# Kernel optimization log

Measured on AMD Instinct MI355X. Metric: run time of the kernel, lower is better.

The kernel has to match this reference:

```python
import jax, jax.numpy as jnp
import numpy as np

B, N, HID, NH = 8, 1024, 1024, 16
HD = HID // NH  # head_dim = 64
MLP = 4 * HID
EPS = 1e-6


def _xavier(key, fan_in, fan_out):
    lim = np.sqrt(6.0 / (fan_in + fan_out))
    return jax.random.uniform(key, (fan_in, fan_out), jnp.float32, -lim, lim)


def setup_inputs() -> dict:
    key = jax.random.key(0)
    ks = jax.random.split(key, 10)
    return {
        "x": jax.random.normal(ks[0], (B, N, HID), jnp.float32),
        "c": jax.random.normal(ks[1], (B, HID), jnp.float32),
        "w_ada": _xavier(ks[2], HID, 6 * HID), "b_ada": jnp.zeros((6 * HID,), jnp.float32),
        "wq": _xavier(ks[3], HID, HID), "bq": jnp.zeros((HID,), jnp.float32),
        "wk": _xavier(ks[4], HID, HID), "bk": jnp.zeros((HID,), jnp.float32),
        "wv": _xavier(ks[5], HID, HID), "bv": jnp.zeros((HID,), jnp.float32),
        "wo": _xavier(ks[6], HID, HID), "bo": jnp.zeros((HID,), jnp.float32),
        "w1": _xavier(ks[7], HID, MLP), "b1": jnp.zeros((MLP,), jnp.float32),
        "w2": _xavier(ks[8], MLP, HID), "b2": jnp.zeros((HID,), jnp.float32),
    }


def _ln(t):
    # LayerNorm, elementwise_affine=False, eps=1e-6
    mu = jnp.mean(t, axis=-1, keepdims=True)
    var = jnp.mean(jnp.square(t - mu), axis=-1, keepdims=True)
    return (t - mu) * jax.lax.rsqrt(var + EPS)


def _modulate(t, shift, scale):
    return t * (1.0 + scale[:, None, :]) + shift[:, None, :]


def reference(x, c, w_ada, b_ada, wq, bq, wk, bk, wv, bv, wo, bo, w1, b1, w2, b2):
    cmod = jax.nn.silu(c) @ w_ada + b_ada  # [B, 6*HID]
    sh_msa, sc_msa, g_msa, sh_mlp, sc_mlp, g_mlp = jnp.split(cmod, 6, axis=-1)

    xm = _modulate(_ln(x), sh_msa, sc_msa)  # [B, N, HID]
    q = (xm @ wq + bq).reshape(B, N, NH, HD)
    k = (xm @ wk + bk).reshape(B, N, NH, HD)
    v = (xm @ wv + bv).reshape(B, N, NH, HD)

    # NOTE: original scales by 1/head_dim (not 1/sqrt(head_dim)), fp32 softmax
    scores = jnp.einsum('bihd,bjhd->bhij', q, k) / HD
    attn = jax.nn.softmax(scores.astype(jnp.float32), axis=-1)
    out = jnp.einsum('bhij,bjhd->bihd', attn, v).astype(v.dtype)
    out = out.reshape(B, N, HID) @ wo + bo

    x = x + g_msa[:, None, :] * out

    xm2 = _modulate(_ln(x), sh_mlp, sc_mlp)
    h = jax.nn.gelu(xm2 @ w1 + b1, approximate=False)  # nn.GELU default = exact
    mlp_out = h @ w2 + b2
    return x + g_mlp[:, None, :] * mlp_out
```

## Files before the change

kernel.cpp:

```cpp
#include <hip/hip_runtime.h>
#include <hip/hip_bf16.h>
#include <cstdint>


typedef __bf16 bf16;
typedef __attribute__((ext_vector_type(8))) __bf16 bf16x8;
typedef __attribute__((ext_vector_type(4))) __bf16 bf16x4;
typedef __attribute__((ext_vector_type(4))) float f32x4;

#define SEQ   1024
#define NHID  1024
#define NHEAD 16
#define HDIM  64
#define CMS   6144

#define GLD16(gp, lp)                                                  \
  __builtin_amdgcn_global_load_lds(                                    \
      (const __attribute__((address_space(1))) void*)(gp),             \
      (__attribute__((address_space(3))) void*)(lp), 16, 0, 0)

template <int N> __device__ __forceinline__ void vmwait() {
  if constexpr (N == 0)      asm volatile("s_waitcnt vmcnt(0)" ::: "memory");
  else if constexpr (N == 3) asm volatile("s_waitcnt vmcnt(3)" ::: "memory");
  else if constexpr (N == 4) asm volatile("s_waitcnt vmcnt(4)" ::: "memory");
  else if constexpr (N == 6) asm volatile("s_waitcnt vmcnt(6)" ::: "memory");
  else                       asm volatile("s_waitcnt vmcnt(8)" ::: "memory");
}

struct TP4 { const float* s[4]; bf16* d[4]; };

__global__ __launch_bounds__(256) void transpose_conv4(TP4 p)
{
  __shared__ float tile[32][33];
  const float* __restrict__ src = p.s[blockIdx.z];
  bf16* __restrict__ dst = p.d[blockIdx.z];
  int n0 = blockIdx.x * 32, k0 = blockIdx.y * 32;
  int tx = threadIdx.x & 31, ty = threadIdx.x >> 5;
#pragma unroll
  for (int i = 0; i < 32; i += 8)
    tile[ty + i][tx] = src[(size_t)(k0 + ty + i) * 1024 + n0 + tx];
  __syncthreads();
#pragma unroll
  for (int i = 0; i < 32; i += 8)
    dst[(size_t)(n0 + ty + i) * 1024 + k0 + tx] = (bf16)tile[tx][ty + i];
}

__global__ __launch_bounds__(256) void transpose_conv(
    const float* __restrict__ src, bf16* __restrict__ dst, int K, int N)
{
  __shared__ float tile[32][33];
  int n0 = blockIdx.x * 32, k0 = blockIdx.y * 32;
  int tx = threadIdx.x & 31, ty = threadIdx.x >> 5;
#pragma unroll
  for (int i = 0; i < 32; i += 8)
    tile[ty + i][tx] = src[(size_t)(k0 + ty + i) * N + n0 + tx];
  __syncthreads();
#pragma unroll
  for (int i = 0; i < 32; i += 8)
    dst[(size_t)(n0 + ty + i) * K + k0 + tx] = (bf16)tile[tx][ty + i];
}

__global__ __launch_bounds__(256) void ada_kernel(
    const float* __restrict__ c, const float* __restrict__ w_ada,
    const float* __restrict__ b_ada, float* __restrict__ cmod)
{
  __shared__ float cs[1024];
  int b = blockIdx.y;
  int col = blockIdx.x * 256 + threadIdx.x;
  for (int i = threadIdx.x; i < 1024; i += 256) {
    float cv = c[b * 1024 + i];
    cs[i] = cv / (1.0f + __expf(-cv));
  }
  __syncthreads();
  float acc = b_ada[col];
#pragma unroll 8
  for (int kk = 0; kk < 1024; kk++)
    acc += cs[kk] * w_ada[(size_t)kk * CMS + col];
  cmod[b * CMS + col] = acc;
}

__global__ __launch_bounds__(256) void ln_mod(
    const float* __restrict__ x, const float* __restrict__ cmod,
    bf16* __restrict__ out, int sh_off, int sc_off)
{
  int row = blockIdx.x, b = row >> 10, tid = threadIdx.x;
  const float4* xr = (const float4*)(x + (size_t)row * NHID);
  float4 v = xr[tid];
  float s  = v.x + v.y + v.z + v.w;
  float s2 = v.x * v.x + v.y * v.y + v.z * v.z + v.w * v.w;
#pragma unroll
  for (int off = 32; off; off >>= 1) {
    s  += __shfl_xor(s, off);
    s2 += __shfl_xor(s2, off);
  }
  __shared__ float red1[4], red2[4];
  int wave = tid >> 6, lane = tid & 63;
  if (lane == 0) { red1[wave] = s; red2[wave] = s2; }
  __syncthreads();
  float S  = red1[0] + red1[1] + red1[2] + red1[3];
  float S2 = red2[0] + red2[1] + red2[2] + red2[3];
  float mean = S * (1.0f / NHID);
  float var  = S2 * (1.0f / NHID) - mean * mean;
  float rs   = rsqrtf(var + 1e-6f);
  const float4* shp = (const float4*)(cmod + b * CMS + sh_off);
  const float4* scp = (const float4*)(cmod + b * CMS + sc_off);
  float4 sh4 = shp[tid], sc4 = scp[tid];
  bf16x4 o4;
  o4[0] = (bf16)((v.x - mean) * rs * (1.0f + sc4.x) + sh4.x);
  o4[1] = (bf16)((v.y - mean) * rs * (1.0f + sc4.y) + sh4.y);
  o4[2] = (bf16)((v.z - mean) * rs * (1.0f + sc4.z) + sh4.z);
  o4[3] = (bf16)((v.w - mean) * rs * (1.0f + sc4.w) + sh4.w);
  *(bf16x4*)(out + (size_t)row * NHID + tid * 4) = o4;
}

template <int EPI, int BN>
__global__ __launch_bounds__(512, 2) void gemm8(
    const bf16* __restrict__ A, const bf16* __restrict__ Bt,
    const float* __restrict__ bias, const float* __restrict__ bias2,
    const float* __restrict__ bias3,
    bf16* __restrict__ outb, bf16* __restrict__ outb2,
    bf16* __restrict__ outb3, float* __restrict__ outf,
    const float* __restrict__ cmod, int gate_off,
    const float* __restrict__ resid,
    int N, int K)
{
  constexpr int BNH   = BN / 2;
  constexpr int LB    = BNH / 64;
  constexpr int NF    = BN / 128;
  constexpr int VMS   = 4 + 2 * LB;
  constexpr int VMF   = 2 + LB;
  constexpr int BOFF  = 65536;
  constexpr int BBUF  = BNH * 256;
  constexpr int BHALF = BNH * 128;

  extern __shared__ __align__(16) char smem[];

  const int tid  = threadIdx.x;
  const int bm = blockIdx.y * 256, bn = blockIdx.x * BN;
  const int wave = tid >> 6, lane = tid & 63;
  const int wr = wave >> 2, wc = wave & 3;
  const int l16 = lane & 15, q4 = lane >> 4;

  const int rq = tid >> 3;
  const int ch = ((tid & 7) ^ (rq & 7)) * 8;
  const int wbase = (tid & 448) * 16;

  const int aRowB = (wr * 64 + l16) * 128;
  const int bRowB = (wc * (BN >> 3) + l16) * 128;
  const int slotB = (q4 ^ (l16 & 7)) * 16;

  f32x4 acc[2][2][4][NF];
#pragma unroll
  for (int a0 = 0; a0 < 2; a0++)
#pragma unroll
    for (int a1 = 0; a1 < 2; a1++)
#pragma unroll
      for (int a2 = 0; a2 < 4; a2++)
#pragma unroll
        for (int a3 = 0; a3 < NF; a3++) acc[a0][a1][a2][a3] = (f32x4)0.0f;

  auto stA = [&](int buf, int half, int T) {
    const bf16* g = A + (size_t)(bm + half * 128 + rq) * K + T * 64 + ch;
    char* l = smem + buf * 32768 + half * 16384 + wbase;
    GLD16(g, l);
    GLD16(g + (size_t)64 * K, l + 8192);
  };
  auto stB = [&](int buf, int half, int T) {
    const bf16* g = Bt + (size_t)(bn + half * BNH + rq) * K + T * 64 + ch;
    char* l = smem + BOFF + buf * BBUF + half * BHALF + wbase;
    GLD16(g, l);
    if constexpr (LB == 2) { GLD16(g + (size_t)64 * K, l + 8192); }
  };

#define PHASE(VMN, BUF, QM, QN, ...)                                       \
  {                                                                        \
    vmwait<VMN>();                                                         \
    __builtin_amdgcn_s_barrier();                                          \
    asm volatile("" ::: "memory");                                         \
    __VA_ARGS__                                                            \
    const char* ab = smem + (BUF) * 32768 + (QM) * 16384 + aRowB;          \
    const char* bb = smem + BOFF + (BUF) * BBUF + (QN) * BHALF + bRowB;    \
    bf16x8 afr[2][4]; bf16x8 bfr[2][NF];                                   \
    _Pragma("unroll")                                                      \
    for (int ks = 0; ks < 2; ks++) {                                       \
      const int sb = slotB ^ (ks * 64);                                    \
      _Pragma("unroll")                                                    \
      for (int mf = 0; mf < 4; mf++)                                       \
        afr[ks][mf] = *(const bf16x8*)(ab + mf * 2048 + sb);               \
      _Pragma("unroll")                                                    \
      for (int nf = 0; nf < NF; nf++)                                      \
        bfr[ks][nf] = *(const bf16x8*)(bb + nf * 2048 + sb);               \
    }                                                                      \
    __builtin_amdgcn_s_setprio(1);                                         \
    _Pragma("unroll")                                                      \
    for (int mf = 0; mf < 4; mf++)                                         \
      _Pragma("unroll")                                                    \
      for (int nf = 0; nf < NF; nf++) {                                    \
        acc[QM][QN][mf][nf] = __builtin_amdgcn_mfma_f32_16x16x32_bf16(     \
            afr[0][mf], bfr[0][nf], acc[QM][QN][mf][nf], 0, 0, 0);         \
        acc[QM][QN][mf][nf] = __builtin_amdgcn_mfma_f32_16x16x32_bf16(     \
            afr[1][mf], bfr[1][nf], acc[QM][QN][mf][nf], 0, 0, 0);         \
      }                                                                    \
    __builtin_amdgcn_s_setprio(0);                                         \
  }

  const int NT = K >> 6, NI = NT >> 1;

  stA(0, 0, 0); stB(0, 0, 0);
  stA(0, 1, 0); stB(0, 1, 0);
  stA(1, 0, 1); stB(1, 0, 1);

  for (int i = 0; i < NI - 1; ++i) {
    const int t = 2 * i;
    PHASE(VMS, 0, 0, 0, stA(1, 1, t + 1); stB(1, 1, t + 1);)
    PHASE(VMS, 0, 0, 1, ;)
    PHASE(VMS, 0, 1, 0, stA(0, 0, t + 2);)
    PHASE(VMS, 0, 1, 1, stB(0, 0, t + 2);)
    PHASE(VMS, 1, 0, 0, stA(0, 1, t + 2); stB(0, 1, t + 2);)
    PHASE(VMS, 1, 0, 1, ;)
    PHASE(VMS, 1, 1, 0, stA(1, 0, t + 3);)
    PHASE(VMS, 1, 1, 1, stB(1, 0, t + 3);)
  }
  {
    const int t = NT - 2;
    PHASE(VMS, 0, 0, 0, stA(1, 1, t + 1); stB(1, 1, t + 1);)
    PHASE(VMS, 0, 0, 1, ;)
    PHASE(VMS, 0, 1, 0, ;)
    PHASE(VMS, 0, 1, 1, ;)
    PHASE(VMF, 1, 0, 0, ;)
    PHASE(0,   1, 0, 1, ;)
    PHASE(0,   1, 1, 0, ;)
    PHASE(0,   1, 1, 1, ;)
  }
#undef PHASE

  const int colBase = bn + wc * (BN >> 3) + l16;
  const int rowBase = bm + wr * 64 + q4 * 4;
#pragma unroll
  for (int qm = 0; qm < 2; qm++)
#pragma unroll
  for (int qn = 0; qn < 2; qn++)
#pragma unroll
  for (int mf = 0; mf < 4; mf++)
#pragma unroll
  for (int nf = 0; nf < NF; nf++) {
    const int col  = colBase + qn * BNH + nf * 16;
    const int row0 = rowBase + qm * 128 + mf * 16;
    f32x4 v = acc[qm][qn][mf][nf];
    if constexpr (EPI == 5) {
      const int sel = bn >> 10;
      const float* bp = (sel == 0) ? bias : (sel == 1) ? bias2 : bias3;
      const int colq = col & 1023;
      const float bcol = bp[colq];
      if (sel == 2) {
        bf16x4 o4;
#pragma unroll
        for (int r = 0; r < 4; r++) o4[r] = (bf16)(v[r] + bcol);
        const int bidx = row0 >> 10;
        *(bf16x4*)(outb3 + ((size_t)bidx * NHID + colq) * SEQ +
                   (row0 & 1023)) = o4;
      } else {
        bf16* qk = (sel == 0) ? outb : outb2;
#pragma unroll
        for (int r = 0; r < 4; r++)
          qk[(size_t)(row0 + r) * 1024 + colq] = (bf16)(v[r] + bcol);
      }
    } else if constexpr (EPI == 2) {
      const float bcol = bias[col];
#pragma unroll
      for (int r = 0; r < 4; r++) {
        float val = v[r] + bcol;
        float u2 = 2.0f * val * (0.7978845608f + 0.0356774081f * val * val);
        float e = __expf(u2);
        float th = 1.0f - 2.0f / (e + 1.0f);
        outb[(size_t)(row0 + r) * N + col] = (bf16)(0.5f * val * (1.0f + th));
      }
    } else {
      const float bcol = bias[col];
#pragma unroll
      for (int r = 0; r < 4; r++) {
        const int row = row0 + r;
        const float gg = cmod[(row >> 10) * CMS + gate_off + col];
        outf[(size_t)row * N + col] =
            resid[(size_t)row * N + col] + gg * (v[r] + bcol);
      }
    }
  }
}

__global__ __launch_bounds__(256) void attn_mfma(
    const bf16* __restrict__ q, const bf16* __restrict__ k,
    const bf16* __restrict__ vt, bf16* __restrict__ o)
{
  __shared__ __align__(16) bf16 Ks[64 * 64];
  __shared__ __align__(16) bf16 Vs[64 * 64];
  __shared__ __align__(16) bf16 Ps[4][32 * 72];

  int bid = blockIdx.x;
  int qt = bid & 7, h = (bid >> 3) & 15, b = bid >> 7;
  int tid = threadIdx.x, wave = tid >> 6, lane = tid & 63;
  int quad = lane >> 4, l16 = lane & 15;
  int qbase = qt * 128 + wave * 32;

  bf16x8 qf[2][2];
  const bf16* qp = q + ((size_t)(b * SEQ + qbase)) * NHID + h * HDIM;
#pragma unroll
  for (int nt = 0; nt < 2; nt++)
#pragma unroll
    for (int kk = 0; kk < 2; kk++) {
      bf16x8 t = *(const bf16x8*)(qp + (size_t)(nt * 16 + l16) * NHID +
                                  kk * 32 + quad * 8);
#pragma unroll
      for (int j = 0; j < 8; j++) t[j] = (bf16)((float)t[j] * 0.015625f);
      qf[nt][kk] = t;
    }

  f32x4 oacc[4][2];
#pragma unroll
  for (int mt = 0; mt < 4; mt++)
#pragma unroll
    for (int nt = 0; nt < 2; nt++) oacc[mt][nt] = (f32x4)0.0f;
  float m_[2] = {-3.0e38f, -3.0e38f}, l_[2] = {0.0f, 0.0f};

  const bf16* kb = k + ((size_t)(b * SEQ)) * NHID + h * HDIM;
  const bf16* vb = vt + ((size_t)(b * NHID + h * HDIM)) * SEQ;

  const int sr0 = tid >> 3, sc0 = tid & 7;

  for (int kt = 0; kt < 16; kt++) {
    __syncthreads();
#pragma unroll
    for (int i = 0; i < 2; i++) {
      int r = i * 32 + sr0;
      int cg = (sc0 ^ (r & 7)) * 8;
      bf16* lk = Ks + (size_t)(i * 256 + (tid & 192)) * 8;
      bf16* lv = Vs + (size_t)(i * 256 + (tid & 192)) * 8;
      GLD16(kb + (size_t)(kt * 64 + r) * NHID + cg, lk);
      GLD16(vb + (size_t)r * SEQ + kt * 64 + cg, lv);
    }
    __syncthreads();

    f32x4 sacc[4][2];
#pragma unroll
    for (int mt = 0; mt < 4; mt++)
#pragma unroll
      for (int nt = 0; nt < 2; nt++) sacc[mt][nt] = (f32x4)0.0f;
#pragma unroll
    for (int kk = 0; kk < 2; kk++) {
      bf16x8 kf[4];
#pragma unroll
      for (int mt = 0; mt < 4; mt++) {
        int row = mt * 16 + l16;
        kf[mt] = *(const bf16x8*)(Ks + row * 64 +
                                  (((kk * 4 + quad) ^ (row & 7)) * 8));
      }
#pragma unroll
      for (int mt = 0; mt < 4; mt++)
#pragma unroll
        for (int nt = 0; nt < 2; nt++)
          sacc[mt][nt] = __builtin_amdgcn_mfma_f32_16x16x32_bf16(
              kf[mt], qf[nt][kk], sacc[mt][nt], 0, 0, 0);
    }

    float alpha[2];
#pragma unroll
    for (int nt = 0; nt < 2; nt++) {
      float tm = -3.0e38f;
#pragma unroll
      for (int mt = 0; mt < 4; mt++)
#pragma unroll
        for (int r = 0; r < 4; r++) tm = fmaxf(tm, sacc[mt][nt][r]);
      tm = fmaxf(tm, __shfl_xor(tm, 16));
      tm = fmaxf(tm, __shfl_xor(tm, 32));
      float mn = fmaxf(m_[nt], tm);
      alpha[nt] = __expf(m_[nt] - mn);
      m_[nt] = mn;
      float ts = 0.0f;
#pragma unroll
      for (int mt = 0; mt < 4; mt++) {
        bf16x4 pv;
#pragma unroll
        for (int r = 0; r < 4; r++) {
          float p = __expf(sacc[mt][nt][r] - mn);
          ts += p;
          pv[r] = (bf16)p;
        }
        *(bf16x4*)(&Ps[wave][(nt * 16 + l16) * 72 + mt * 16 + quad * 4]) = pv;
      }
      ts += __shfl_xor(ts, 16);
      ts += __shfl_xor(ts, 32);
      l_[nt] = l_[nt] * alpha[nt] + ts;
    }
#pragma unroll
    for (int mt = 0; mt < 4; mt++)
#pragma unroll
      for (int nt = 0; nt < 2; nt++)
#pragma unroll
        for (int r = 0; r < 4; r++) oacc[mt][nt][r] *= alpha[nt];

    __asm__ volatile("s_waitcnt lgkmcnt(0)" ::: "memory");

#pragma unroll
    for (int kk = 0; kk < 2; kk++) {
      bf16x8 vf[4], pf[2];
#pragma unroll
      for (int mt = 0; mt < 4; mt++) {
        int row = mt * 16 + l16;
        vf[mt] = *(const bf16x8*)(Vs + row * 64 +
                                  (((kk * 4 + quad) ^ (row & 7)) * 8));
      }
#pragma unroll
      for (int nt = 0; nt < 2; nt++)
        pf[nt] = *(const bf16x8*)(&Ps[wave][(nt * 16 + l16) * 72 +
                                            kk * 32 + quad * 8]);
#pragma unroll
      for (int mt = 0; mt < 4; mt++)
#pragma unroll
        for (int nt = 0; nt < 2; nt++)
          oacc[mt][nt] = __builtin_amdgcn_mfma_f32_16x16x32_bf16(
              vf[mt], pf[nt], oacc[mt][nt], 0, 0, 0);
    }
  }

#pragma unroll
  for (int nt = 0; nt < 2; nt++) {
    float rl = 1.0f / l_[nt];
#pragma unroll
    for (int mt = 0; mt < 4; mt++) {
      bf16x4 o4;
#pragma unroll
      for (int r = 0; r < 4; r++) o4[r] = (bf16)(oacc[mt][nt][r] * rl);
      *(bf16x4*)(o + ((size_t)(b * SEQ + qbase + nt * 16 + l16)) * NHID +
                 h * HDIM + mt * 16 + quad * 4) = o4;
    }
  }
}

#define OFF_CMOD 0u
#define OFF_WQT  196608u
#define OFF_WKT  (OFF_WQT + 2097152u)
#define OFF_WVT  (OFF_WKT + 2097152u)
#define OFF_WOT  (OFF_WVT + 2097152u)
#define OFF_W1T  (OFF_WOT + 2097152u)
#define OFF_W2T  (OFF_W1T + 8388608u)
#define OFF_X2   (OFF_W2T + 8388608u)
#define OFF_XM2  (OFF_X2  + 33554432u)
#define OFF_POOL (OFF_XM2 + 16777216u)

extern "C" void kernel_launch(void* const* d_in, const int* in_sizes, int n_in,
                              void* d_out, int out_size, void* d_ws, size_t ws_size,
                              hipStream_t stream)
{
  const float* x     = (const float*)d_in[0];
  const float* c     = (const float*)d_in[1];
  const float* w_ada = (const float*)d_in[2];
  const float* b_ada = (const float*)d_in[3];
  const float* wq = (const float*)d_in[4];  const float* bq = (const float*)d_in[5];
  const float* wk = (const float*)d_in[6];  const float* bk = (const float*)d_in[7];
  const float* wv = (const float*)d_in[8];  const float* bv = (const float*)d_in[9];
  const float* wo = (const float*)d_in[10]; const float* bo = (const float*)d_in[11];
  const float* w1 = (const float*)d_in[12]; const float* b1 = (const float*)d_in[13];
  const float* w2 = (const float*)d_in[14]; const float* b2 = (const float*)d_in[15];
  float* out = (float*)d_out;
  char* ws = (char*)d_ws;

  float* cmod = (float*)(ws + OFF_CMOD);
  bf16* wqT = (bf16*)(ws + OFF_WQT);
  bf16* wkT = (bf16*)(ws + OFF_WKT);
  bf16* wvT = (bf16*)(ws + OFF_WVT);
  bf16* woT = (bf16*)(ws + OFF_WOT);
  bf16* w1T = (bf16*)(ws + OFF_W1T);
  bf16* w2T = (bf16*)(ws + OFF_W2T);
  float* x2 = (float*)(ws + OFF_X2);
  bf16* xm2 = (bf16*)(ws + OFF_XM2);
  bf16* xm  = (bf16*)(ws + OFF_POOL);
  bf16* qb  = (bf16*)(ws + OFF_POOL + 16777216u);
  bf16* kb  = (bf16*)(ws + OFF_POOL + 33554432u);
  bf16* vtb = (bf16*)(ws + OFF_POOL + 50331648u);
  bf16* ob  = xm;
  bf16* hb  = xm;

  static bool attr_set = false;
  if (!attr_set) {
    hipFuncSetAttribute(reinterpret_cast<const void*>(&gemm8<5, 128>),
                        hipFuncAttributeMaxDynamicSharedMemorySize, 131072);
    hipFuncSetAttribute(reinterpret_cast<const void*>(&gemm8<1, 128>),
                        hipFuncAttributeMaxDynamicSharedMemorySize, 131072);
    hipFuncSetAttribute(reinterpret_cast<const void*>(&gemm8<2, 256>),
                        hipFuncAttributeMaxDynamicSharedMemorySize, 131072);
    hipFuncSetAttribute(reinterpret_cast<const void*>(&gemm8<3, 128>),
                        hipFuncAttributeMaxDynamicSharedMemorySize, 131072);
    attr_set = true;
  }

  TP4 tp;
  tp.s[0] = wq; tp.s[1] = wk; tp.s[2] = wv; tp.s[3] = wo;
  tp.d[0] = wqT; tp.d[1] = wkT; tp.d[2] = wvT; tp.d[3] = woT;
  transpose_conv4<<<dim3(32, 32, 4), 256, 0, stream>>>(tp);
  transpose_conv<<<dim3(128, 32), 256, 0, stream>>>(w1, w1T, 1024, 4096);
  transpose_conv<<<dim3(32, 128), 256, 0, stream>>>(w2, w2T, 4096, 1024);

  ada_kernel<<<dim3(24, 8), 256, 0, stream>>>(c, w_ada, b_ada, cmod);

  ln_mod<<<8192, 256, 0, stream>>>(x, cmod, xm, 0, 1024);

  gemm8<5, 128><<<dim3(24, 32), 512, 98304, stream>>>(
      xm, wqT, bq, bk, bv, qb, kb, vtb, nullptr, nullptr, 0, nullptr,
      1024, 1024);

  attn_mfma<<<1024, 256, 0, stream>>>(qb, kb, vtb, ob);

  gemm8<1, 128><<<dim3(8, 32), 512, 98304, stream>>>(
      ob, woT, bo, nullptr, nullptr, nullptr, nullptr, nullptr, x2,
      cmod, 2048, x, 1024, 1024);

  ln_mod<<<8192, 256, 0, stream>>>(x2, cmod, xm2, 3072, 4096);

  gemm8<2, 256><<<dim3(16, 32), 512, 131072, stream>>>(
      xm2, w1T, b1, nullptr, nullptr, hb, nullptr, nullptr, nullptr,
      nullptr, 0, nullptr, 4096, 1024);

  gemm8<3, 128><<<dim3(8, 32), 512, 98304, stream>>>(
      hb, w2T, b2, nullptr, nullptr, nullptr, nullptr, nullptr, out,
      cmod, 5120, x2, 1024, 4096);
}
```

Measured before the change: 616.6 us.

## Restructure GEMM main loop to reuse LDS fragments across quadrants and relayout waves

Rewrites the gemm8 pipeline so that A and B fragments read from LDS are reused across consecutive quadrant MFMA groups (0,0 -> 0,1 -> 1,1 -> 1,0), which cuts LDS reads per tile. Prefetch stores now go out between the compute quadrants of a single uniform loop, replacing the peeled tail. The wave grid changes to BN/64 columns, giving each wave 32 columns and MF rows. To keep the loop uniform, the last iterations issue dummy loads of tile 0. This adds redundant global traffic and changes the vmcnt accounting, and the dynamic shared memory attribute for the BN=128 variants is lowered to 98304.

```diff
diff --git a/kernel.cpp b/kernel.cpp
--- a/kernel.cpp
+++ b/kernel.cpp
@@ -21,11 +21,14 @@
 
 template <int N> __device__ __forceinline__ void vmwait() {
   if constexpr (N == 0)      asm volatile("s_waitcnt vmcnt(0)" ::: "memory");
-  else if constexpr (N == 3) asm volatile("s_waitcnt vmcnt(3)" ::: "memory");
-  else if constexpr (N == 4) asm volatile("s_waitcnt vmcnt(4)" ::: "memory");
+  else if constexpr (N == 5) asm volatile("s_waitcnt vmcnt(5)" ::: "memory");
   else if constexpr (N == 6) asm volatile("s_waitcnt vmcnt(6)" ::: "memory");
-  else                       asm volatile("s_waitcnt vmcnt(8)" ::: "memory");
-}
+}
+
+#define BAR()                                                          \
+  { asm volatile("" ::: "memory");                                     \
+    __builtin_amdgcn_s_barrier();                                      \
+    asm volatile("" ::: "memory"); }
 
 struct TP4 { const float* s[4]; bf16* d[4]; };
 
@@ -126,9 +129,10 @@
 {
   constexpr int BNH   = BN / 2;
   constexpr int LB    = BNH / 64;
-  constexpr int NF    = BN / 128;
-  constexpr int VMS   = 4 + 2 * LB;
-  constexpr int VMF   = 2 + LB;
+  constexpr int MF    = BN / 64;
+  constexpr int WC    = BN / 64;
+  constexpr int WRS   = MF * 16;
+  constexpr int VMN   = (LB == 2) ? 6 : 5;
   constexpr int BOFF  = 65536;
   constexpr int BBUF  = BNH * 256;
   constexpr int BHALF = BNH * 128;
@@ -138,26 +142,26 @@
   const int tid  = threadIdx.x;
   const int bm = blockIdx.y * 256, bn = blockIdx.x * BN;
   const int wave = tid >> 6, lane = tid & 63;
-  const int wr = wave >> 2, wc = wave & 3;
+  const int wr = wave / WC, wc = wave % WC;
   const int l16 = lane & 15, q4 = lane >> 4;
 
   const int rq = tid >> 3;
   const int ch = ((tid & 7) ^ (rq & 7)) * 8;
   const int wbase = (tid & 448) * 16;
 
-  const int aRowB = (wr * 64 + l16) * 128;
-  const int bRowB = (wc * (BN >> 3) + l16) * 128;
+  const int aRowB = (wr * WRS + l16) * 128;
+  const int bRowB = (wc * 32 + l16) * 128;
   const int slotB = (q4 ^ (l16 & 7)) * 16;
 
-  f32x4 acc[2][2][4][NF];
+  f32x4 acc[2][2][MF][2];
 #pragma unroll
   for (int a0 = 0; a0 < 2; a0++)
 #pragma unroll
     for (int a1 = 0; a1 < 2; a1++)
 #pragma unroll
-      for (int a2 = 0; a2 < 4; a2++)
-#pragma unroll
-        for (int a3 = 0; a3 < NF; a3++) acc[a0][a1][a2][a3] = (f32x4)0.0f;
+      for (int a2 = 0; a2 < MF; a2++)
+#pragma unroll
+        for (int a3 = 0; a3 < 2; a3++) acc[a0][a1][a2][a3] = (f32x4)0.0f;
 
   auto stA = [&](int buf, int half, int T) {
     const bf16* g = A + (size_t)(bm + half * 128 + rq) * K + T * 64 + ch;
@@ -172,78 +176,94 @@
     if constexpr (LB == 2) { GLD16(g + (size_t)64 * K, l + 8192); }
   };
 
-#define PHASE(VMN, BUF, QM, QN, ...)                                       \
-  {                                                                        \
-    vmwait<VMN>();                                                         \
-    __builtin_amdgcn_s_barrier();                                          \
-    asm volatile("" ::: "memory");                                         \
-    __VA_ARGS__                                                            \
-    const char* ab = smem + (BUF) * 32768 + (QM) * 16384 + aRowB;          \
-    const char* bb = smem + BOFF + (BUF) * BBUF + (QN) * BHALF + bRowB;    \
-    bf16x8 afr[2][4]; bf16x8 bfr[2][NF];                                   \
+#define RDA(BUF, QM, FR)                                                   \
+  { const char* ab_ = smem + (BUF) * 32768 + (QM) * 16384 + aRowB;         \
     _Pragma("unroll")                                                      \
     for (int ks = 0; ks < 2; ks++) {                                       \
-      const int sb = slotB ^ (ks * 64);                                    \
+      const int sb_ = slotB ^ (ks * 64);                                   \
       _Pragma("unroll")                                                    \
-      for (int mf = 0; mf < 4; mf++)                                       \
-        afr[ks][mf] = *(const bf16x8*)(ab + mf * 2048 + sb);               \
+      for (int mf = 0; mf < MF; mf++)                                      \
+        FR[ks][mf] = *(const bf16x8*)(ab_ + mf * 2048 + sb_);              \
+    } }
+
+#define RDB(BUF, QN, FR)                                                   \
+  { const char* bb_ = smem + BOFF + (BUF) * BBUF + (QN) * BHALF + bRowB;   \
+    _Pragma("unroll")                                                      \
+    for (int ks = 0; ks < 2; ks++) {                                       \
+      const int sb_ = slotB ^ (ks * 64);                                   \
       _Pragma("unroll")                                                    \
-      for (int nf = 0; nf < NF; nf++)                                      \
-        bfr[ks][nf] = *(const bf16x8*)(bb + nf * 2048 + sb);               \
-    }                                                                      \
-    __builtin_amdgcn_s_setprio(1);                                         \
+      for (int nf = 0; nf < 2; nf++)                                       \
+        FR[ks][nf] = *(const bf16x8*)(bb_ + nf * 2048 + sb_);              \
+    } }
+
+#define MM(QM, QN, AF, BF)                                                 \
+  { __builtin_amdgcn_s_setprio(1);                                         \
     _Pragma("unroll")                                                      \
-    for (int mf = 0; mf < 4; mf++)                                         \
+    for (int mf = 0; mf < MF; mf++)                                        \
       _Pragma("unroll")                                                    \
-      for (int nf = 0; nf < NF; nf++) {                                    \
+      for (int nf = 0; nf < 2; nf++) {                                     \
         acc[QM][QN][mf][nf] = __builtin_amdgcn_mfma_f32_16x16x32_bf16(     \
-            afr[0][mf], bfr[0][nf], acc[QM][QN][mf][nf], 0, 0, 0);         \
+            AF[0][mf], BF[0][nf], acc[QM][QN][mf][nf], 0, 0, 0);           \
         acc[QM][QN][mf][nf] = __builtin_amdgcn_mfma_f32_16x16x32_bf16(     \
-            afr[1][mf], bfr[1][nf], acc[QM][QN][mf][nf], 0, 0, 0);         \
+            AF[1][mf], BF[1][nf], acc[QM][QN][mf][nf], 0, 0, 0);           \
       }                                                                    \
-    __builtin_amdgcn_s_setprio(0);                                         \
-  }
+    __builtin_amdgcn_s_setprio(0); }
 
   const int NT = K >> 6, NI = NT >> 1;
 
-  stA(0, 0, 0); stB(0, 0, 0);
-  stA(0, 1, 0); stB(0, 1, 0);
-  stA(1, 0, 1); stB(1, 0, 1);
-
-  for (int i = 0; i < NI - 1; ++i) {
+  bf16x8 afr[2][MF], bfr0[2][2], bfr1[2][2];
+
+  stA(0, 0, 0); stB(0, 0, 0); stB(0, 1, 0); stA(0, 1, 0);
+  stA(1, 0, 1); stB(1, 0, 1); stB(1, 1, 1); stA(1, 1, 1);
+
+  for (int i = 0; i < NI; ++i) {
     const int t = 2 * i;
-    PHASE(VMS, 0, 0, 0, stA(1, 1, t + 1); stB(1, 1, t + 1);)
-    PHASE(VMS, 0, 0, 1, ;)
-    PHASE(VMS, 0, 1, 0, stA(0, 0, t + 2);)
-    PHASE(VMS, 0, 1, 1, stB(0, 0, t + 2);)
-    PHASE(VMS, 1, 0, 0, stA(0, 1, t + 2); stB(0, 1, t + 2);)
-    PHASE(VMS, 1, 0, 1, ;)
-    PHASE(VMS, 1, 1, 0, stA(1, 0, t + 3);)
-    PHASE(VMS, 1, 1, 1, stB(1, 0, t + 3);)
-  }
-  {
-    const int t = NT - 2;
-    PHASE(VMS, 0, 0, 0, stA(1, 1, t + 1); stB(1, 1, t + 1);)
-    PHASE(VMS, 0, 0, 1, ;)
-    PHASE(VMS, 0, 1, 0, ;)
-    PHASE(VMS, 0, 1, 1, ;)
-    PHASE(VMF, 1, 0, 0, ;)
-    PHASE(0,   1, 0, 1, ;)
-    PHASE(0,   1, 1, 0, ;)
-    PHASE(0,   1, 1, 1, ;)
-  }
-#undef PHASE
-
-  const int colBase = bn + wc * (BN >> 3) + l16;
-  const int rowBase = bm + wr * 64 + q4 * 4;
+    const int u2 = (t + 2 < NT) ? t + 2 : 0;
+    const int u3 = (t + 3 < NT) ? t + 3 : 0;
+    vmwait<VMN>(); BAR();
+    RDA(0, 0, afr); RDB(0, 0, bfr0);
+    MM(0, 0, afr, bfr0);
+    BAR();
+    RDB(0, 1, bfr1);
+    stA(0, 0, u2); stB(0, 0, u2);
+    MM(0, 1, afr, bfr1);
+    BAR();
+    RDA(0, 1, afr);
+    stB(0, 1, u2);
+    MM(1, 1, afr, bfr1);
+    BAR();
+    stA(0, 1, u2);
+    MM(1, 0, afr, bfr0);
+    vmwait<VMN>(); BAR();
+    RDA(1, 0, afr); RDB(1, 0, bfr0);
+    MM(0, 0, afr, bfr0);
+    BAR();
+    RDB(1, 1, bfr1);
+    stA(1, 0, u3); stB(1, 0, u3);
+    MM(0, 1, afr, bfr1);
+    BAR();
+    RDA(1, 1, afr);
+    stB(1, 1, u3);
+    MM(1, 1, afr, bfr1);
+    BAR();
+    stA(1, 1, u3);
+    MM(1, 0, afr, bfr0);
+  }
+  vmwait<0>();
+#undef RDA
+#undef RDB
+#undef MM
+
+  const int colBase = bn + wc * 32 + l16;
+  const int rowBase = bm + wr * WRS + q4 * 4;
 #pragma unroll
   for (int qm = 0; qm < 2; qm++)
 #pragma unroll
   for (int qn = 0; qn < 2; qn++)
 #pragma unroll
-  for (int mf = 0; mf < 4; mf++)
-#pragma unroll
-  for (int nf = 0; nf < NF; nf++) {
+  for (int mf = 0; mf < MF; mf++)
+#pragma unroll
+  for (int nf = 0; nf < 2; nf++) {
     const int col  = colBase + qn * BNH + nf * 16;
     const int row0 = rowBase + qm * 128 + mf * 16;
     f32x4 v = acc[qm][qn][mf][nf];
@@ -270,8 +290,8 @@
 #pragma unroll
       for (int r = 0; r < 4; r++) {
         float val = v[r] + bcol;
-        float u2 = 2.0f * val * (0.7978845608f + 0.0356774081f * val * val);
-        float e = __expf(u2);
+        float u2g = 2.0f * val * (0.7978845608f + 0.0356774081f * val * val);
+        float e = __expf(u2g);
         float th = 1.0f - 2.0f / (e + 1.0f);
         outb[(size_t)(row0 + r) * N + col] = (bf16)(0.5f * val * (1.0f + th));
       }
@@ -483,13 +503,13 @@
   static bool attr_set = false;
   if (!attr_set) {
     hipFuncSetAttribute(reinterpret_cast<const void*>(&gemm8<5, 128>),
-                        hipFuncAttributeMaxDynamicSharedMemorySize, 131072);
+                        hipFuncAttributeMaxDynamicSharedMemorySize, 98304);
     hipFuncSetAttribute(reinterpret_cast<const void*>(&gemm8<1, 128>),
-                        hipFuncAttributeMaxDynamicSharedMemorySize, 131072);
+                        hipFuncAttributeMaxDynamicSharedMemorySize, 98304);
     hipFuncSetAttribute(reinterpret_cast<const void*>(&gemm8<2, 256>),
                         hipFuncAttributeMaxDynamicSharedMemorySize, 131072);
     hipFuncSetAttribute(reinterpret_cast<const void*>(&gemm8<3, 128>),
-                        hipFuncAttributeMaxDynamicSharedMemorySize, 131072);
+                        hipFuncAttributeMaxDynamicSharedMemorySize, 98304);
     attr_set = true;
   }
 
```

After: 579.3 us. 6.1% less time.
